# Performance work log

Measured on AMD Instinct MI355X. Metric: run time of the kernel, lower is better.

The kernel has to match this reference:

```python
import jax, jax.numpy as jnp
import numpy as np

SIGMA_AGG = 0.5
SIGMA_DIS = 3.0
ALPHA = 0.5
BETA = 0.25
EPS = 1e-5
K_MAX = 8  # number of kernel/text instances per image; labels in {0..K_MAX}, 0 = background


def setup_inputs() -> dict:
    key = jax.random.key(0)
    ks = jax.random.split(key, 7)
    B, C, H, W = 16, 4, 640, 640
    return dict(
        pred_regions=jax.random.normal(ks[0], (B, 1, H, W), jnp.float32),
        regions_gt=jax.random.randint(ks[1], (B, 1, H, W), 0, 2).astype(jnp.float32),
        pred_kernels=jax.random.normal(ks[2], (B, 1, H, W), jnp.float32),
        kernels_gt=jax.random.randint(ks[3], (B, 1, H, W), 0, 2).astype(jnp.float32),
        pred_similarities=jax.random.normal(ks[4], (B, C, H, W), jnp.float32),
        text_mask_ndi_labels=jax.random.randint(ks[5], (B, H, W), 0, K_MAX + 1, dtype=jnp.int32),
        kernel_mask_ndi_labels=jax.random.randint(ks[6], (B, H, W), 0, K_MAX + 1, dtype=jnp.int32),
    )


def _dice_loss(pred, gt, eps):
    # sigmoid -> per-sample dice, summed over batch (matches Text/KernelDiceLoss)
    p = jax.nn.sigmoid(pred).reshape(pred.shape[0], -1)
    g = gt.reshape(gt.shape[0], -1)
    inter = jnp.sum(p * g, axis=1)
    denom = (jnp.sum(p * p, axis=1) + eps) + (jnp.sum(g * g, axis=1) + eps)
    dice = (2.0 * inter + eps) / denom
    return jnp.sum(1.0 - dice)


def _agg_dis_single(sim, tlab, klab):
    # sim: (C, H, W); tlab/klab: (H, W) int instance labels (0 = background)
    C = sim.shape[0]
    sim = sim.reshape(C, -1)
    tlab = tlab.reshape(-1)
    klab = klab.reshape(-1)
    nseg = K_MAX + 1

    s2 = jnp.sum(sim * sim, axis=0)  # per-pixel squared feature norm, (N,)
    ones = jnp.ones_like(s2)
    ck = jax.ops.segment_sum(ones, klab, num_segments=nseg)  # kernel cardinalities
    ct = jax.ops.segment_sum(ones, tlab, num_segments=nseg)  # text cardinalities

    # Aggregation: || sim*1[T==i] - sim*1[K==i]/(ck_i+1) ||_F per instance i.
    # Per pixel, nonzero only for i = tlab[p] or i = klab[p]:
    inv = 1.0 / (ck + 1.0)
    same = tlab == klab
    coef_t = jnp.where(same, (1.0 - inv[klab]) ** 2, 1.0)  # contributes to instance tlab
    coef_k = jnp.where(same, 0.0, inv[klab] ** 2)          # contributes to instance klab
    n2 = (jax.ops.segment_sum(s2 * coef_t, tlab, num_segments=nseg)
          + jax.ops.segment_sum(s2 * coef_k, klab, num_segments=nseg))
    norm = jnp.sqrt(n2[1:])  # drop background segment 0
    # NOTE: torch.max(scalar, 0)[0] on a 0-d tensor is identity (no clamp) - reproduced here.
    l_agg = jnp.sum(jnp.log((norm - SIGMA_AGG) ** 2 + 1.0) / (ct[1:] + 1.0))

    # Discrimination: kernel masks are disjoint, so
    # ||mu_i - mu_j||_F^2 = a_i + a_j with a_i = sum_{K==i} s2 / (ck_i + 0.001)^2
    a = jax.ops.segment_sum(s2, klab, num_segments=nseg)[1:] / (ck[1:] + 0.001) ** 2
    pair = SIGMA_DIS - jnp.sqrt(a[:, None] + a[None, :])
    val = jnp.log(pair ** 2 + 1.0)
    triu = jnp.triu(jnp.ones((K_MAX, K_MAX), bool), 1)
    l_dis = jnp.sum(jnp.where(triu, val, 0.0)) / (K_MAX * (K_MAX - 1))
    return l_agg, l_dis


def reference(pred_regions, regions_gt, pred_kernels, kernels_gt,
              pred_similarities, text_mask_ndi_labels, kernel_mask_ndi_labels):
    # OHEM mask is computed in the torch code but never used by TextDiceLoss, so it is omitted.
    loss_regions = _dice_loss(pred_regions, regions_gt, EPS)
    loss_kernel = _dice_loss(pred_kernels, kernels_gt, EPS)
    l_agg, l_dis = jax.vmap(_agg_dis_single)(pred_similarities,
                                             text_mask_ndi_labels,
                                             kernel_mask_ndi_labels)
    loss_aggregation = jnp.sum(l_agg)
    loss_discrimination = jnp.sum(l_dis)
    loss = loss_regions + ALPHA * loss_kernel + BETA * (loss_aggregation + loss_discrimination)
    return (loss, loss_regions, loss_kernel, loss_aggregation, loss_discrimination)
```

## Files before the change

### kernel.cpp

```cpp
#include <hip/hip_runtime.h>
#include <math.h>


#define NSEG 9
#define NACC 51
#define NBATCH 16
#define EPSF 1e-5f
#define BPB 400

typedef float  vfloat4 __attribute__((ext_vector_type(4)));
typedef int    vint4   __attribute__((ext_vector_type(4)));

__device__ __forceinline__ float wave_reduce_sum(float v) {
#pragma unroll
    for (int off = 32; off > 0; off >>= 1)
        v += __shfl_down(v, off, 64);
    return v;
}

__device__ __forceinline__ float sigm(float x) {
    return 1.0f / (1.0f + __expf(-x));
}

__device__ __forceinline__ vfloat4 nt_load4(const float* p) {
    return __builtin_nontemporal_load((const vfloat4*)p);
}
__device__ __forceinline__ vint4 nt_load4i(const int* p) {
    return __builtin_nontemporal_load((const vint4*)p);
}

__global__ __launch_bounds__(256) void pan_main(
    const float* __restrict__ pred_r, const float* __restrict__ gt_r,
    const float* __restrict__ pred_k, const float* __restrict__ gt_k,
    const float* __restrict__ sim,
    const int* __restrict__ tlab, const int* __restrict__ klab,
    float* __restrict__ ws, int npix)
{
    const int tid = threadIdx.x;
    const int b = blockIdx.y;
    const int i = blockIdx.x * 256 + tid;
    const long long e = (long long)i * 4;
    const long long base = (long long)b * npix;
    const long long sbase = (long long)b * 4 * npix;

    const vfloat4 pr = nt_load4(pred_r + base + e);
    const vfloat4 gr = nt_load4(gt_r + base + e);
    const vfloat4 pk = nt_load4(pred_k + base + e);
    const vfloat4 gk = nt_load4(gt_k + base + e);
    const vfloat4 c0 = nt_load4(sim + sbase + e);
    const vfloat4 c1 = nt_load4(sim + sbase + npix + e);
    const vfloat4 c2 = nt_load4(sim + sbase + 2LL * npix + e);
    const vfloat4 c3 = nt_load4(sim + sbase + 3LL * npix + e);
    const vint4 tl = nt_load4i(tlab + base + e);
    const vint4 kl = nt_load4i(klab + base + e);

    float rpg, rpp, rgg, kpg, kpp, kgg;
    {
        float p;
        p = sigm(pr.x); rpg  = p * gr.x; rpp  = p * p; rgg  = gr.x;
        p = sigm(pr.y); rpg += p * gr.y; rpp += p * p; rgg += gr.y;
        p = sigm(pr.z); rpg += p * gr.z; rpp += p * p; rgg += gr.z;
        p = sigm(pr.w); rpg += p * gr.w; rpp += p * p; rgg += gr.w;
        p = sigm(pk.x); kpg  = p * gk.x; kpp  = p * p; kgg  = gk.x;
        p = sigm(pk.y); kpg += p * gk.y; kpp += p * p; kgg += gk.y;
        p = sigm(pk.z); kpg += p * gk.z; kpp += p * p; kgg += gk.z;
        p = sigm(pk.w); kpg += p * gk.w; kpp += p * p; kgg += gk.w;
    }

    const float s2x = c0.x * c0.x + c1.x * c1.x + c2.x * c2.x + c3.x * c3.x;
    const float s2y = c0.y * c0.y + c1.y * c1.y + c2.y * c2.y + c3.y * c3.y;
    const float s2z = c0.z * c0.z + c1.z * c1.z + c2.z * c2.z + c3.z * c3.z;
    const float s2w = c0.w * c0.w + c1.w * c1.w + c2.w * c2.w + c3.w * c3.w;

    float St_[8], Sk_[8], Ss_[8];
    unsigned ct_[8], ck_[8];

#define DO_COMP(TL, KL, S2, OP)                                      \
    {                                                                \
        bool tt = ((TL) == s);                                       \
        bool kk = ((KL) == s);                                       \
        ct_[s - 1] OP (unsigned)__popcll(__ballot(tt));              \
        ck_[s - 1] OP (unsigned)__popcll(__ballot(kk));              \
        St_[s - 1] OP tt ? (S2) : 0.0f;                              \
        Sk_[s - 1] OP kk ? (S2) : 0.0f;                              \
        Ss_[s - 1] OP (tt && kk) ? (S2) : 0.0f;                      \
    }

#pragma unroll
    for (int s = 1; s <= 8; ++s) {
        DO_COMP(tl.x, kl.x, s2x, =);
        DO_COMP(tl.y, kl.y, s2y, +=);
        DO_COMP(tl.z, kl.z, s2z, +=);
        DO_COMP(tl.w, kl.w, s2w, +=);
    }
#undef DO_COMP

    __shared__ float red[4][NACC];
    const int lane = tid & 63;
    const int wv = tid >> 6;

#pragma unroll
    for (int s = 0; s < 8; ++s) {
        float v;
        v = wave_reduce_sum(St_[s]); if (lane == 0) red[wv][19 + s] = v;
        v = wave_reduce_sum(Sk_[s]); if (lane == 0) red[wv][28 + s] = v;
        v = wave_reduce_sum(Ss_[s]); if (lane == 0) red[wv][37 + s] = v;
    }
    {
        float v;
        v = wave_reduce_sum(rpg); if (lane == 0) red[wv][45] = v;
        v = wave_reduce_sum(rpp); if (lane == 0) red[wv][46] = v;
        v = wave_reduce_sum(rgg); if (lane == 0) red[wv][47] = v;
        v = wave_reduce_sum(kpg); if (lane == 0) red[wv][48] = v;
        v = wave_reduce_sum(kpp); if (lane == 0) red[wv][49] = v;
        v = wave_reduce_sum(kgg); if (lane == 0) red[wv][50] = v;
    }
    if (lane == 0) {
#pragma unroll
        for (int s = 0; s < 8; ++s) {
            red[wv][1 + s] = (float)ct_[s];
            red[wv][10 + s] = (float)ck_[s];
        }
        red[wv][0] = 0.0f; red[wv][9] = 0.0f; red[wv][18] = 0.0f;
        red[wv][27] = 0.0f; red[wv][36] = 0.0f;
    }
    __syncthreads();
    if (tid < NACC) {
        float s = red[0][tid] + red[1][tid] + red[2][tid] + red[3][tid];
        atomicAdd(&ws[b * NACC + tid], s);
    }
}

__global__ __launch_bounds__(64) void pan_finalize(
    const float* __restrict__ ws, float* __restrict__ out)
{
    const int b = threadIdx.x;
    float dice_r = 0.0f, dice_k = 0.0f, lagg = 0.0f, ldis = 0.0f;

    if (b < NBATCH) {
        const float* w = ws + b * NACC;
        {
            float pg = w[45], pp = w[46], gg = w[47];
            dice_r = 1.0f - (2.0f * pg + EPSF) / ((pp + EPSF) + (gg + EPSF));
            pg = w[48]; pp = w[49]; gg = w[50];
            dice_k = 1.0f - (2.0f * pg + EPSF) / ((pp + EPSF) + (gg + EPSF));
        }
        float a[8];
#pragma unroll
        for (int i = 1; i < NSEG; ++i) {
            float ct = w[i], ck = w[NSEG + i];
            float St = w[2 * NSEG + i], Sk = w[3 * NSEG + i], Ss = w[4 * NSEG + i];
            float inv = 1.0f / (ck + 1.0f);
            float omi = 1.0f - inv;
            float n2 = omi * omi * Ss + (St - Ss) + inv * inv * (Sk - Ss);
            float nrm = sqrtf(n2);
            float d = nrm - 0.5f;
            lagg += logf(d * d + 1.0f) / (ct + 1.0f);
            float ckd = ck + 0.001f;
            a[i - 1] = Sk / (ckd * ckd);
        }
#pragma unroll
        for (int i = 0; i < 8; ++i) {
#pragma unroll
            for (int j = i + 1; j < 8; ++j) {
                float pair = 3.0f - sqrtf(a[i] + a[j]);
                ldis += logf(pair * pair + 1.0f);
            }
        }
        ldis *= (1.0f / 56.0f);
    }

    dice_r = wave_reduce_sum(dice_r);
    dice_k = wave_reduce_sum(dice_k);
    lagg = wave_reduce_sum(lagg);
    ldis = wave_reduce_sum(ldis);

    if (threadIdx.x == 0) {
        float loss = dice_r + 0.5f * dice_k + 0.25f * (lagg + ldis);
        out[0] = loss;
        out[1] = dice_r;
        out[2] = dice_k;
        out[3] = lagg;
        out[4] = ldis;
    }
}

extern "C" void kernel_launch(void* const* d_in, const int* in_sizes, int n_in,
                              void* d_out, int out_size, void* d_ws, size_t ws_size,
                              hipStream_t stream) {
    const float* pred_r = (const float*)d_in[0];
    const float* gt_r   = (const float*)d_in[1];
    const float* pred_k = (const float*)d_in[2];
    const float* gt_k   = (const float*)d_in[3];
    const float* sim    = (const float*)d_in[4];
    const int*   tlab   = (const int*)d_in[5];
    const int*   klab   = (const int*)d_in[6];
    float* out = (float*)d_out;
    float* ws  = (float*)d_ws;

    const int npix = in_sizes[0] / NBATCH;

    (void)hipMemsetAsync(ws, 0, NBATCH * NACC * sizeof(float), stream);

    dim3 grid(BPB, NBATCH);
    pan_main<<<grid, 256, 0, stream>>>(pred_r, gt_r, pred_k, gt_k, sim,
                                       tlab, klab, ws, npix);
    pan_finalize<<<1, 64, 0, stream>>>(ws, out);
}
```

Measured before the change: 282.1 us.

## Replace per-segment ballot/shuffle reductions with shared-memory atomic histograms

Swaps the unrolled 8-segment compare, ballot and wave-shuffle reductions for direct shared-memory float atomics indexed by the label, building a per-block histogram of counts and squared-norm sums. The aim is to cut the large number of shuffle reductions and registers per thread. In exchange, LDS atomics on only 9 bins per group suffer heavy contention, and background label 0 is now accumulated too but never read.

```diff
diff --git a/kernel.cpp b/kernel.cpp
--- a/kernel.cpp
+++ b/kernel.cpp
@@ -36,7 +36,11 @@
     const int* __restrict__ tlab, const int* __restrict__ klab,
     float* __restrict__ ws, int npix)
 {
+    __shared__ float h[NACC];
     const int tid = threadIdx.x;
+    if (tid < NACC) h[tid] = 0.0f;
+    __syncthreads();
+
     const int b = blockIdx.y;
     const int i = blockIdx.x * 256 + tid;
     const long long e = (long long)i * 4;
@@ -72,63 +76,37 @@
     const float s2z = c0.z * c0.z + c1.z * c1.z + c2.z * c2.z + c3.z * c3.z;
     const float s2w = c0.w * c0.w + c1.w * c1.w + c2.w * c2.w + c3.w * c3.w;
 
-    float St_[8], Sk_[8], Ss_[8];
-    unsigned ct_[8], ck_[8];
+#define DO_COMP(TL, KL, S2)                                   \
+    {                                                         \
+        atomicAdd(&h[(TL)], 1.0f);                            \
+        atomicAdd(&h[9 + (KL)], 1.0f);                        \
+        atomicAdd(&h[18 + (TL)], (S2));                       \
+        atomicAdd(&h[27 + (KL)], (S2));                       \
+        if ((TL) == (KL)) atomicAdd(&h[36 + (TL)], (S2));     \
+    }
+    DO_COMP(tl.x, kl.x, s2x);
+    DO_COMP(tl.y, kl.y, s2y);
+    DO_COMP(tl.z, kl.z, s2z);
+    DO_COMP(tl.w, kl.w, s2w);
+#undef DO_COMP
 
-#define DO_COMP(TL, KL, S2, OP)                                      \
-    {                                                                \
-        bool tt = ((TL) == s);                                       \
-        bool kk = ((KL) == s);                                       \
-        ct_[s - 1] OP (unsigned)__popcll(__ballot(tt));              \
-        ck_[s - 1] OP (unsigned)__popcll(__ballot(kk));              \
-        St_[s - 1] OP tt ? (S2) : 0.0f;                              \
-        Sk_[s - 1] OP kk ? (S2) : 0.0f;                              \
-        Ss_[s - 1] OP (tt && kk) ? (S2) : 0.0f;                      \
+    rpg = wave_reduce_sum(rpg);
+    rpp = wave_reduce_sum(rpp);
+    rgg = wave_reduce_sum(rgg);
+    kpg = wave_reduce_sum(kpg);
+    kpp = wave_reduce_sum(kpp);
+    kgg = wave_reduce_sum(kgg);
+    if ((tid & 63) == 0) {
+        atomicAdd(&h[45], rpg);
+        atomicAdd(&h[46], rpp);
+        atomicAdd(&h[47], rgg);
+        atomicAdd(&h[48], kpg);
+        atomicAdd(&h[49], kpp);
+        atomicAdd(&h[50], kgg);
     }
 
-#pragma unroll
-    for (int s = 1; s <= 8; ++s) {
-        DO_COMP(tl.x, kl.x, s2x, =);
-        DO_COMP(tl.y, kl.y, s2y, +=);
-        DO_COMP(tl.z, kl.z, s2z, +=);
-        DO_COMP(tl.w, kl.w, s2w, +=);
-    }
-#undef DO_COMP
-
-    __shared__ float red[4][NACC];
-    const int lane = tid & 63;
-    const int wv = tid >> 6;
-
-#pragma unroll
-    for (int s = 0; s < 8; ++s) {
-        float v;
-        v = wave_reduce_sum(St_[s]); if (lane == 0) red[wv][19 + s] = v;
-        v = wave_reduce_sum(Sk_[s]); if (lane == 0) red[wv][28 + s] = v;
-        v = wave_reduce_sum(Ss_[s]); if (lane == 0) red[wv][37 + s] = v;
-    }
-    {
-        float v;
-        v = wave_reduce_sum(rpg); if (lane == 0) red[wv][45] = v;
-        v = wave_reduce_sum(rpp); if (lane == 0) red[wv][46] = v;
-        v = wave_reduce_sum(rgg); if (lane == 0) red[wv][47] = v;
-        v = wave_reduce_sum(kpg); if (lane == 0) red[wv][48] = v;
-        v = wave_reduce_sum(kpp); if (lane == 0) red[wv][49] = v;
-        v = wave_reduce_sum(kgg); if (lane == 0) red[wv][50] = v;
-    }
-    if (lane == 0) {
-#pragma unroll
-        for (int s = 0; s < 8; ++s) {
-            red[wv][1 + s] = (float)ct_[s];
-            red[wv][10 + s] = (float)ck_[s];
-        }
-        red[wv][0] = 0.0f; red[wv][9] = 0.0f; red[wv][18] = 0.0f;
-        red[wv][27] = 0.0f; red[wv][36] = 0.0f;
-    }
     __syncthreads();
-    if (tid < NACC) {
-        float s = red[0][tid] + red[1][tid] + red[2][tid] + red[3][tid];
-        atomicAdd(&ws[b * NACC + tid], s);
-    }
+    if (tid < NACC) atomicAdd(&ws[b * NACC + tid], h[tid]);
 }
 
 __global__ __launch_bounds__(64) void pan_finalize(
```

New measurement: 364.1 us. 29.1% more time.
